# Optimization experiments

Hardware: AMD Instinct MI355X
Metric: run time of the kernel (lower is better)

## Reference

```python
import jax, jax.numpy as jnp
import numpy as np

B, C, H, W = 2, 256, 48, 48
HIDDEN, NUM_HEADS = 512, 8
HEAD_DIM = HIDDEN // NUM_HEADS
EPS = 1e-5


def setup_inputs() -> dict:
    key = jax.random.key(0)
    ks = jax.random.split(key, 16)
    inp = {
        'modal1_feat': jax.random.normal(ks[0], (B, C, H, W), jnp.float32),
        'modal2_feat': jax.random.normal(ks[1], (B, C, H, W), jnp.float32),
    }
    s = 0.02  # weight init scale
    names = ['wq1', 'wk1', 'wv1', 'wq2', 'wk2', 'wv2']
    for i, nm in enumerate(names):
        inp[nm] = jax.random.normal(ks[2 + i], (HIDDEN, C), jnp.float32) * s
        inp['b' + nm[1:]] = jnp.zeros((HIDDEN,), jnp.float32)
    inp['wo1'] = jax.random.normal(ks[8], (C, HIDDEN), jnp.float32) * s
    inp['bo1'] = jnp.zeros((C,), jnp.float32)
    inp['wo2'] = jax.random.normal(ks[9], (C, HIDDEN), jnp.float32) * s
    inp['bo2'] = jnp.zeros((C,), jnp.float32)
    inp['ln1_g'] = jnp.ones((C,), jnp.float32)
    inp['ln1_b'] = jnp.zeros((C,), jnp.float32)
    inp['ln2_g'] = jnp.ones((C,), jnp.float32)
    inp['ln2_b'] = jnp.zeros((C,), jnp.float32)
    inp['wf'] = jax.random.normal(ks[10], (C, 2 * C), jnp.float32) * s
    inp['bf'] = jnp.zeros((C,), jnp.float32)
    inp['bn_g'] = jnp.ones((C,), jnp.float32)
    inp['bn_b'] = jnp.zeros((C,), jnp.float32)
    inp['bn_mean'] = jnp.zeros((C,), jnp.float32)
    inp['bn_var'] = jnp.ones((C,), jnp.float32)
    return inp


def _conv1x1(x, w, b):
    return jnp.einsum('bchw,oc->bohw', x, w) + b[None, :, None, None]


def _ln_channels(x, g, b):
    # LayerNorm over channel dim (x: [B,C,H,W]) applied in NHWC layout
    xc = x.transpose(0, 2, 3, 1)
    mu = xc.mean(-1, keepdims=True)
    var = ((xc - mu) ** 2).mean(-1, keepdims=True)
    y = (xc - mu) / jnp.sqrt(var + EPS) * g + b
    return y.transpose(0, 3, 1, 2)


def reference(modal1_feat, modal2_feat, wq1, bq1, wk1, bk1, wv1, bv1,
              wq2, bq2, wk2, bk2, wv2, bv2, wo1, bo1, wo2, bo2,
              ln1_g, ln1_b, ln2_g, ln2_b, wf, bf, bn_g, bn_b, bn_mean, bn_var):
    b_, c1, h1, w1 = modal1_feat.shape
    hw = h1 * w1
    scale = HEAD_DIM ** -0.5

    def as_q(t):  # [B,hidden,H,W] -> [B,h,L,d]
        return t.reshape(b_, NUM_HEADS, HEAD_DIM, hw).transpose(0, 1, 3, 2)

    def as_k(t):  # [B,h,d,L]
        return t.reshape(b_, NUM_HEADS, HEAD_DIM, hw)

    q1 = as_q(_conv1x1(modal1_feat, wq1, bq1))
    k1 = as_k(_conv1x1(modal1_feat, wk1, bk1))
    v1 = as_q(_conv1x1(modal1_feat, wv1, bv1))
    q2 = as_q(_conv1x1(modal2_feat, wq2, bq2))
    k2 = as_k(_conv1x1(modal2_feat, wk2, bk2))
    v2 = as_q(_conv1x1(modal2_feat, wv2, bv2))

    a12 = jax.nn.softmax(jnp.einsum('bhld,bhdm->bhlm', q1, k2) * scale, axis=-1)
    o1 = jnp.einsum('bhlm,bhmd->bhld', a12, v2).transpose(0, 1, 3, 2).reshape(b_, HIDDEN, h1, w1)
    a21 = jax.nn.softmax(jnp.einsum('bhld,bhdm->bhlm', q2, k1) * scale, axis=-1)
    o2 = jnp.einsum('bhlm,bhmd->bhld', a21, v1).transpose(0, 1, 3, 2).reshape(b_, HIDDEN, h1, w1)

    mod1_cross = _conv1x1(o1, wo1, bo1)
    mod2_cross = _conv1x1(o2, wo2, bo2)

    m1 = _ln_channels(modal1_feat + mod1_cross, ln1_g, ln1_b)
    m2 = _ln_channels(modal2_feat + mod2_cross, ln2_g, ln2_b)

    fused = jnp.concatenate([m1, m2], axis=1)
    f = _conv1x1(fused, wf, bf)
    # BatchNorm2d in eval mode (running stats)
    f = (f - bn_mean[None, :, None, None]) / jnp.sqrt(bn_var + EPS)[None, :, None, None]
    f = f * bn_g[None, :, None, None] + bn_b[None, :, None, None]
    return jax.nn.relu(f)
```

## Files before the change

kernel.cpp:

```cpp
#include <hip/hip_runtime.h>
#include <hip/hip_bf16.h>

#define HW_N 2304
#define EPS_F 1e-5f
#define QSCALE 0.18033688011112043f

typedef float f32x4 __attribute__((ext_vector_type(4)));
typedef float f32x16 __attribute__((ext_vector_type(16)));
typedef unsigned u32x4 __attribute__((ext_vector_type(4)));
typedef short short8v __attribute__((ext_vector_type(8)));
typedef __bf16 bf16x8 __attribute__((ext_vector_type(8)));
typedef unsigned short u16;

__device__ __forceinline__ f32x4 mfma_bf16(bf16x8 a, bf16x8 b, f32x4 c) {
    return __builtin_amdgcn_mfma_f32_16x16x32_bf16(a, b, c, 0, 0, 0);
}
__device__ __forceinline__ f32x16 mfma32(bf16x8 a, bf16x8 b, f32x16 c) {
    return __builtin_amdgcn_mfma_f32_32x32x16_bf16(a, b, c, 0, 0, 0);
}
__device__ __forceinline__ bf16x8 ld8(const void* p) {
    return __builtin_bit_cast(bf16x8, *(const short8v*)p);
}
__device__ __forceinline__ unsigned short bfbits(float v) {
    return __builtin_bit_cast(unsigned short, __float2bfloat16(v));
}
__device__ __forceinline__ float b2f(u16 u) {
    unsigned x = (unsigned)u << 16;
    return __builtin_bit_cast(float, x);
}
__device__ __forceinline__ unsigned pack2(float lo, float hi) {
    return (unsigned)bfbits(lo) | ((unsigned)bfbits(hi) << 16);
}
__device__ __forceinline__ f32x16 zero16() {
    f32x16 z;
#pragma unroll
    for (int i = 0; i < 16; ++i) z[i] = 0.f;
    return z;
}

struct WPtrs { const float* s[9]; u16* d[9]; };

__global__ __launch_bounds__(256)
void conv_w_kernel(WPtrs p)
{
    const int j = blockIdx.z;
    const float* s = p.s[j];
    u16* d = p.d[j];
    const int i = (blockIdx.x * 256 + threadIdx.x) * 4;
    const float4 v = *(const float4*)(s + i);
    ushort4 pk;
    pk.x = bfbits(v.x); pk.y = bfbits(v.y); pk.z = bfbits(v.z); pk.w = bfbits(v.w);
    *(ushort4*)(d + i) = pk;
}

__global__ __launch_bounds__(256)
void prep_modal_kernel(const float* __restrict__ m1, const float* __restrict__ m2,
                       u16* __restrict__ t1, u16* __restrict__ t2)
{
    const int l0 = blockIdx.x * 64, c0 = blockIdx.y * 64;
    const int which = blockIdx.z >> 1, b = blockIdx.z & 1;
    const float* src = (which ? m2 : m1) + ((long long)b * 256 + c0) * HW_N + l0;
    u16* dst = (which ? t2 : t1) + ((long long)b * HW_N + l0) * 256 + c0;

    __shared__ float tile[64][65];
    const int t = threadIdx.x;
    const int r = t >> 4, cq = (t & 15) * 4;
#pragma unroll
    for (int i = 0; i < 4; ++i) {
        const int row = r + i * 16;
        const float4 v = *(const float4*)(src + (long long)row * HW_N + cq);
        tile[row][cq + 0] = v.x; tile[row][cq + 1] = v.y;
        tile[row][cq + 2] = v.z; tile[row][cq + 3] = v.w;
    }
    __syncthreads();
#pragma unroll
    for (int i = 0; i < 4; ++i) {
        const int lr = r + i * 16;
        ushort4 pk;
        pk.x = bfbits(tile[cq + 0][lr]);
        pk.y = bfbits(tile[cq + 1][lr]);
        pk.z = bfbits(tile[cq + 2][lr]);
        pk.w = bfbits(tile[cq + 3][lr]);
        *(ushort4*)(dst + (long long)lr * 256 + cq) = pk;
    }
}

struct GArgs {
    const u16* W[6];
    const float* bias[6];
    const u16* X[2];
    const u16* R[2];
    u16* outQ[2]; u16* outK[2]; u16* outV[2];
    float* outT[2];
    float* outC;
    const float *bnm, *bnv, *bng, *bnb;
};

template<int MODE>
__global__ __launch_bounds__(256)
void gemm_mfma(GArgs g)
{
    constexpr int KD = (MODE == 0) ? 256 : 512;
    constexpr int NS = KD / 32;
    const int z = blockIdx.y;
    const int j = blockIdx.z;
    const int mt_b = blockIdx.x / 18;
    const int nt_b = blockIdx.x - mt_b * 18;
    const int m0 = mt_b * 128, n0 = nt_b * 128;

    const u16* Wb = g.W[(MODE == 2) ? 0 : j];
    const u16* Xb0 = (MODE == 0) ? g.X[(j < 3) ? 0 : 1]
                                 : ((MODE == 1) ? g.X[j] : nullptr);

    __shared__ u16 Als[4096];
    __shared__ u16 Bls[4096];

    const int tid = threadIdx.x;
    const int w = tid >> 6, lane = tid & 63;
    const int l16 = lane & 15, lg = lane >> 4;

    const int ar0 = (((tid >> 6) << 4) | (tid & 15));
    const int k8 = (tid >> 4) & 3;

    short8v sa0, sa1, sb0, sb1;

    auto stage = [&](int kb) {
        const int koff = kb + k8 * 8;
        sa0 = *(const short8v*)(Wb + (long long)(m0 + ar0) * KD + koff);
        sa1 = *(const short8v*)(Wb + (long long)(m0 + ar0 + 64) * KD + koff);
        if constexpr (MODE == 0) {
            const u16* p = Xb0 + ((long long)z * HW_N + n0 + ar0) * 256 + koff;
            sb0 = *(const short8v*)p;
            sb1 = *(const short8v*)(p + 64LL * 256);
        } else if constexpr (MODE == 1) {
            const int head = kb >> 6;
            const u16* p = Xb0 + (((long long)z * 8 + head) * HW_N + n0 + ar0) * 64 + (koff & 63);
            sb0 = *(const short8v*)p;
            sb1 = *(const short8v*)(p + 64LL * 64);
        } else {
            const u16* Xb = (kb < 256) ? g.X[0] : g.X[1];
            const u16* p = Xb + ((long long)z * HW_N + n0 + ar0) * 256 + (koff & 255);
            sb0 = *(const short8v*)p;
            sb1 = *(const short8v*)(p + 64LL * 256);
        }
    };

    f32x4 acc[4][4];
#pragma unroll
    for (int a = 0; a < 4; ++a)
#pragma unroll
        for (int b = 0; b < 4; ++b) acc[a][b] = f32x4{0.f, 0.f, 0.f, 0.f};

    stage(0);
    for (int s = 0; s < NS; ++s) {
        __syncthreads();
        *(short8v*)((char*)Als + tid * 16) = sa0;
        *(short8v*)((char*)Als + tid * 16 + 4096) = sa1;
        *(short8v*)((char*)Bls + tid * 16) = sb0;
        *(short8v*)((char*)Bls + tid * 16 + 4096) = sb1;
        __syncthreads();
        if (s + 1 < NS) stage((s + 1) * 32);

        bf16x8 bfr[4];
#pragma unroll
        for (int nt = 0; nt < 4; ++nt)
            bfr[nt] = ld8((char*)Bls + ((w & 1) * 4 + nt) * 1024 + lane * 16);
#pragma unroll
        for (int mt = 0; mt < 4; ++mt) {
            const bf16x8 af = ld8((char*)Als + ((w >> 1) * 4 + mt) * 1024 + lane * 16);
#pragma unroll
            for (int nt = 0; nt < 4; ++nt)
                acc[mt][nt] = mfma_bf16(af, bfr[nt], acc[mt][nt]);
        }
    }

    const int mbase = m0 + (w >> 1) * 64 + 4 * lg;
    const int nbase = n0 + (w & 1) * 64 + l16;

    if constexpr (MODE == 0) {
        const int kind = j % 3, which = j / 3;
        const float* Bp = g.bias[j];
        if (kind < 2) {
            u16* T = (kind == 0) ? g.outQ[which] : g.outK[which];
            const float s = (kind == 0) ? QSCALE : 1.0f;
#pragma unroll
            for (int mt = 0; mt < 4; ++mt) {
                const int m = mbase + mt * 16;
                const float4 bv = *(const float4*)(Bp + m);
#pragma unroll
                for (int nt = 0; nt < 4; ++nt) {
                    const int l = nbase + nt * 16;
                    const f32x4 a = acc[mt][nt];
                    ushort4 pk;
                    pk.x = bfbits((a.x + bv.x) * s);
                    pk.y = bfbits((a.y + bv.y) * s);
                    pk.z = bfbits((a.z + bv.z) * s);
                    pk.w = bfbits((a.w + bv.w) * s);
                    *(ushort4*)(T + ((long long)(z * 8 + (m >> 6)) * HW_N + l) * 64 + (m & 63)) = pk;
                }
            }
        } else {
            u16* V = g.outV[which];
#pragma unroll
            for (int mt = 0; mt < 4; ++mt) {
                const int m = mbase + mt * 16;
                const float4 bv = *(const float4*)(Bp + m);
#pragma unroll
                for (int nt = 0; nt < 4; ++nt) {
                    const int l = nbase + nt * 16;
                    const f32x4 a = acc[mt][nt];
                    V[((long long)z * 512 + m + 0) * HW_N + l] = bfbits(a.x + bv.x);
                    V[((long long)z * 512 + m + 1) * HW_N + l] = bfbits(a.y + bv.y);
                    V[((long long)z * 512 + m + 2) * HW_N + l] = bfbits(a.z + bv.z);
                    V[((long long)z * 512 + m + 3) * HW_N + l] = bfbits(a.w + bv.w);
                }
            }
        }
    } else if constexpr (MODE == 1) {
        const float* Bp = g.bias[j];
        const u16* Rb = g.R[j];
        float* Ob = g.outT[j];
#pragma unroll
        for (int mt = 0; mt < 4; ++mt) {
            const int m = mbase + mt * 16;
            const float4 bv = *(const float4*)(Bp + m);
#pragma unroll
            for (int nt = 0; nt < 4; ++nt) {
                const int l = nbase + nt * 16;
                const long long rowoff = ((long long)z * HW_N + l) * 256 + m;
                const ushort4 rv = *(const ushort4*)(Rb + rowoff);
                const f32x4 a = acc[mt][nt];
                float4 o;
                o.x = a.x + bv.x + b2f(rv.x);
                o.y = a.y + bv.y + b2f(rv.y);
                o.z = a.z + bv.z + b2f(rv.z);
                o.w = a.w + bv.w + b2f(rv.w);
                *(float4*)(Ob + rowoff) = o;
            }
        }
    } else {
        const float* Bp = g.bias[0];
#pragma unroll
        for (int mt = 0; mt < 4; ++mt) {
            const int m = mbase + mt * 16;
            const float4 bv = *(const float4*)(Bp + m);
            const float4 mu = *(const float4*)(g.bnm + m);
            const float4 vr = *(const float4*)(g.bnv + m);
            const float4 ga = *(const float4*)(g.bng + m);
            const float4 be = *(const float4*)(g.bnb + m);
            const float sc0 = ga.x * rsqrtf(vr.x + EPS_F), sh0 = be.x - mu.x * sc0;
            const float sc1 = ga.y * rsqrtf(vr.y + EPS_F), sh1 = be.y - mu.y * sc1;
            const float sc2 = ga.z * rsqrtf(vr.z + EPS_F), sh2 = be.z - mu.z * sc2;
            const float sc3 = ga.w * rsqrtf(vr.w + EPS_F), sh3 = be.w - mu.w * sc3;
#pragma unroll
            for (int nt = 0; nt < 4; ++nt) {
                const int l = nbase + nt * 16;
                const f32x4 a = acc[mt][nt];
                float* O = g.outC + (long long)z * 256 * HW_N + l;
                O[(long long)(m + 0) * HW_N] = fmaxf((a.x + bv.x) * sc0 + sh0, 0.f);
                O[(long long)(m + 1) * HW_N] = fmaxf((a.y + bv.y) * sc1 + sh1, 0.f);
                O[(long long)(m + 2) * HW_N] = fmaxf((a.z + bv.z) * sc2 + sh2, 0.f);
                O[(long long)(m + 3) * HW_N] = fmaxf((a.w + bv.w) * sc3 + sh3, 0.f);
            }
        }
    }
}

__global__ __launch_bounds__(256)
void attn_mfma_kernel(const u16* __restrict__ qt0, const u16* __restrict__ kt0,
                      const u16* __restrict__ v0b,
                      const u16* __restrict__ qt1, const u16* __restrict__ kt1,
                      const u16* __restrict__ v1b,
                      u16* __restrict__ oat0T, u16* __restrict__ oat1T)
{
    const int flat = blockIdx.x;
    const int virt = (flat & 7) * 72 + (flat >> 3);
    const int lt = virt % 18;
    const int hz = virt / 18;
    const int h = hz & 7;
    const int zz = hz >> 3;
    const int b = zz >> 1, dir = zz & 1;

    const u16* QT = dir ? qt1 : qt0;
    const u16* KT = dir ? kt0 : kt1;
    const u16* V  = dir ? v0b : v1b;

    const long long bh = (long long)(b * 8 + h);
    const u16* Qb = QT + bh * HW_N * 64;
    const u16* Kb = KT + bh * HW_N * 64;
    const u16* Vb = V + ((long long)b * 512 + h * 64) * HW_N;

    const int tid = threadIdx.x;
    const int w = tid >> 6, lane = tid & 63;
    const int l32 = lane & 31, hi = lane >> 5;
    const int q0 = lt * 128 + w * 32;

    __shared__ u16 Ks[2][64 * 64];
    __shared__ u16 Vs[2][64 * 64];

    bf16x8 qf0, qf1, qf2, qf3;
    {
        const u16* qrow = Qb + (long long)(q0 + l32) * 64 + 8 * hi;
        qf0 = ld8(qrow);       qf1 = ld8(qrow + 16);
        qf2 = ld8(qrow + 32);  qf3 = ld8(qrow + 48);
    }
    bf16x8 onesv;
    {
        short8v o;
#pragma unroll
        for (int i = 0; i < 8; ++i) o[i] = (short)0x3F80;
        onesv = __builtin_bit_cast(bf16x8, o);
    }

    f32x16 accA = zero16(), accB = zero16(), accs = zero16();
    float m_run = -1e30f;

    auto SWZ = [](int r) { return ((r ^ (r >> 3)) & 7) << 4; };

    const int rsub = lane >> 3;
    const int csub = (lane & 7) * 8;
    const int r0 = 16 * w + rsub, r1 = r0 + 8;
    const int swz0 = (csub * 2) ^ SWZ(r0);
    const int swz1 = (csub * 2) ^ SWZ(r1);

    short8v ka, kb2, va, vb2;
    auto stage = [&](int t) {
        const int m0 = t * 64;
        const u16* kbase = Kb + (long long)(m0 + 16 * w) * 64;
        ka  = *(const short8v*)(kbase + (long long)rsub * 64 + csub);
        kb2 = *(const short8v*)(kbase + (long long)(8 + rsub) * 64 + csub);
        const u16* vbase = Vb + (long long)(16 * w + rsub) * HW_N + m0 + csub;
        va  = *(const short8v*)(vbase);
        vb2 = *(const short8v*)(vbase + 8LL * HW_N);
    };
    auto commit = [&](int buf) {
        *(short8v*)((char*)Ks[buf] + r0 * 128 + swz0) = ka;
        *(short8v*)((char*)Ks[buf] + r1 * 128 + swz1) = kb2;
        *(short8v*)((char*)Vs[buf] + r0 * 128 + swz0) = va;
        *(short8v*)((char*)Vs[buf] + r1 * 128 + swz1) = vb2;
    };

    const int rb0 = l32 * 128;
    const int rb1 = (l32 + 32) * 128;
    const int cs0 = (16 * hi) ^ SWZ(l32);
    const int cs1 = (16 * hi) ^ SWZ(l32 + 32);

    stage(0); commit(0); stage(1);
    __syncthreads();

    for (int t = 0; t < 36; ++t) {
        const int cur = t & 1;
        const char* kbase = (const char*)Ks[cur];
        const char* vbase = (const char*)Vs[cur];

        const bf16x8 kf00 = ld8(kbase + rb0 + (cs0 ^ 0));
        const bf16x8 kf01 = ld8(kbase + rb1 + (cs1 ^ 0));
        const bf16x8 kf10 = ld8(kbase + rb0 + (cs0 ^ 32));
        const bf16x8 kf11 = ld8(kbase + rb1 + (cs1 ^ 32));
        const bf16x8 kf20 = ld8(kbase + rb0 + (cs0 ^ 64));
        const bf16x8 kf21 = ld8(kbase + rb1 + (cs1 ^ 64));
        const bf16x8 kf30 = ld8(kbase + rb0 + (cs0 ^ 96));
        const bf16x8 kf31 = ld8(kbase + rb1 + (cs1 ^ 96));

        if (t + 1 < 36) commit(cur ^ 1);
        if (t + 2 < 36) stage(t + 2);

        f32x16 s0 = zero16(), s1 = zero16();
        __builtin_amdgcn_s_setprio(1);
        s0 = mfma32(kf00, qf0, s0); s1 = mfma32(kf01, qf0, s1);
        s0 = mfma32(kf10, qf1, s0); s1 = mfma32(kf11, qf1, s1);
        s0 = mfma32(kf20, qf2, s0); s1 = mfma32(kf21, qf2, s1);
        s0 = mfma32(kf30, qf3, s0); s1 = mfma32(kf31, qf3, s1);
        __builtin_amdgcn_s_setprio(0);

        const bf16x8 vf00 = ld8(vbase + rb0 + (cs0 ^ 0));
        const bf16x8 vf01 = ld8(vbase + rb1 + (cs1 ^ 0));
        const bf16x8 vf10 = ld8(vbase + rb0 + (cs0 ^ 32));
        const bf16x8 vf11 = ld8(vbase + rb1 + (cs1 ^ 32));
        const bf16x8 vf20 = ld8(vbase + rb0 + (cs0 ^ 64));
        const bf16x8 vf21 = ld8(vbase + rb1 + (cs1 ^ 64));
        const bf16x8 vf30 = ld8(vbase + rb0 + (cs0 ^ 96));
        const bf16x8 vf31 = ld8(vbase + rb1 + (cs1 ^ 96));

        f32x16 mv;
#pragma unroll
        for (int i = 0; i < 16; ++i) mv[i] = fmaxf(s0[i], s1[i]);
        float ma = fmaxf(fmaxf(mv[0], mv[1]), fmaxf(mv[2], mv[3]));
        float mb = fmaxf(fmaxf(mv[4], mv[5]), fmaxf(mv[6], mv[7]));
        float mc = fmaxf(fmaxf(mv[8], mv[9]), fmaxf(mv[10], mv[11]));
        float md = fmaxf(fmaxf(mv[12], mv[13]), fmaxf(mv[14], mv[15]));
        float mx = fmaxf(fmaxf(ma, mb), fmaxf(mc, md));
        {
            unsigned mu = __builtin_bit_cast(unsigned, mx);
            unsigned mv2 = mu;
            asm("v_permlane32_swap_b32 %0, %1" : "+v"(mu), "+v"(mv2));
            mx = fmaxf(__builtin_bit_cast(float, mu), __builtin_bit_cast(float, mv2));
        }

        if (!__all(mx <= m_run + 8.f)) {
            const float m_new = fmaxf(m_run, mx);
            const float alpha = exp2f(m_run - m_new);
#pragma unroll
            for (int i = 0; i < 16; ++i) {
                accA[i] *= alpha; accB[i] *= alpha; accs[i] *= alpha;
            }
            m_run = m_new;
        }

#pragma unroll
        for (int i = 0; i < 16; ++i) {
            s0[i] = exp2f(s0[i] - m_run);
            s1[i] = exp2f(s1[i] - m_run);
        }

        __builtin_amdgcn_s_setprio(1);
#define PVSTEP(S, PT, VF0, VF1) { \
        constexpr int qe = 2 * ((S) & 1), qo = qe + 1; \
        unsigned a0 = pack2(PT[4 * qe + 0], PT[4 * qe + 1]); \
        unsigned b0 = pack2(PT[4 * qe + 2], PT[4 * qe + 3]); \
        unsigned a1 = pack2(PT[4 * qo + 0], PT[4 * qo + 1]); \
        unsigned b1 = pack2(PT[4 * qo + 2], PT[4 * qo + 3]); \
        asm("v_permlane32_swap_b32 %0, %1" : "+v"(a0), "+v"(a1)); \
        asm("v_permlane32_swap_b32 %0, %1" : "+v"(b0), "+v"(b1)); \
        u32x4 pw = {a0, b0, a1, b1}; \
        const bf16x8 pf = __builtin_bit_cast(bf16x8, pw); \
        accA = mfma32(VF0, pf, accA); \
        accB = mfma32(VF1, pf, accB); \
        accs = mfma32(onesv, pf, accs); }
        PVSTEP(0, s0, vf00, vf01)
        PVSTEP(1, s0, vf10, vf11)
        PVSTEP(2, s1, vf20, vf21)
        PVSTEP(3, s1, vf30, vf31)
#undef PVSTEP
        __builtin_amdgcn_s_setprio(0);

        __syncthreads();
    }

    const float inv = 1.0f / accs[0];
    u16* obase = (dir ? oat1T : oat0T) + (bh * HW_N + q0 + l32) * 64;
#pragma unroll
    for (int g = 0; g < 4; ++g) {
        ushort4 pk;
        pk.x = bfbits(accA[4 * g + 0] * inv);
        pk.y = bfbits(accA[4 * g + 1] * inv);
        pk.z = bfbits(accA[4 * g + 2] * inv);
        pk.w = bfbits(accA[4 * g + 3] * inv);
        *(ushort4*)(obase + 8 * g + 4 * hi) = pk;
        pk.x = bfbits(accB[4 * g + 0] * inv);
        pk.y = bfbits(accB[4 * g + 1] * inv);
        pk.z = bfbits(accB[4 * g + 2] * inv);
        pk.w = bfbits(accB[4 * g + 3] * inv);
        *(ushort4*)(obase + 32 + 8 * g + 4 * hi) = pk;
    }
}

__global__ __launch_bounds__(256)
void ln_t_kernel(const float* __restrict__ mpre0T, const float* __restrict__ mpre1T,
                 const float* __restrict__ g1, const float* __restrict__ b1,
                 const float* __restrict__ g2, const float* __restrict__ b2,
                 u16* __restrict__ mln0T, u16* __restrict__ mln1T)
{
    const int l = blockIdx.x * 64 + (threadIdx.x >> 2);
    const int z = blockIdx.y, dir = blockIdx.z;
    const float* src = (dir ? mpre1T : mpre0T) + ((long long)z * HW_N + l) * 256;
    const float* gg = dir ? g2 : g1;
    const float* bb = dir ? b2 : b1;
    u16* dst = (dir ? mln1T : mln0T) + ((long long)z * HW_N + l) * 256;
    const int q = (threadIdx.x & 3) * 64;

    float4 vbuf[16];
    float sum = 0.f, sq = 0.f;
#pragma unroll
    for (int i = 0; i < 16; ++i) {
        const float4 v = *(const float4*)(src + q + i * 4);
        vbuf[i] = v;
        sum += (v.x + v.y) + (v.z + v.w);
        sq += (v.x * v.x + v.y * v.y) + (v.z * v.z + v.w * v.w);
    }
    sum += __shfl_xor(sum, 1, 64); sum += __shfl_xor(sum, 2, 64);
    sq  += __shfl_xor(sq, 1, 64);  sq  += __shfl_xor(sq, 2, 64);
    const float mean = sum * (1.f / 256.f);
    const float var = sq * (1.f / 256.f) - mean * mean;
    const float rstd = rsqrtf(var + EPS_F);
#pragma unroll
    for (int i = 0; i < 16; ++i) {
        const int c = q + i * 4;
        const float4 gv = *(const float4*)(gg + c);
        const float4 bv = *(const float4*)(bb + c);
        ushort4 pk;
        pk.x = bfbits((vbuf[i].x - mean) * rstd * gv.x + bv.x);
        pk.y = bfbits((vbuf[i].y - mean) * rstd * gv.y + bv.y);
        pk.z = bfbits((vbuf[i].z - mean) * rstd * gv.z + bv.z);
        pk.w = bfbits((vbuf[i].w - mean) * rstd * gv.w + bv.w);
        *(ushort4*)(dst + c) = pk;
    }
}

extern "C" void kernel_launch(void* const* d_in, const int* in_sizes, int n_in,
                              void* d_out, int out_size, void* d_ws, size_t ws_size,
                              hipStream_t stream)
{
    (void)in_sizes; (void)n_in; (void)out_size; (void)ws_size;

    const float* modal1 = (const float*)d_in[0];
    const float* modal2 = (const float*)d_in[1];
    const float* wqkv[6]; const float* bqkv[6];
    for (int j = 0; j < 6; ++j) {
        wqkv[j] = (const float*)d_in[2 + 2 * j];
        bqkv[j] = (const float*)d_in[3 + 2 * j];
    }
    const float* wo1 = (const float*)d_in[14];
    const float* bo1 = (const float*)d_in[15];
    const float* wo2 = (const float*)d_in[16];
    const float* bo2 = (const float*)d_in[17];
    const float* ln1_g = (const float*)d_in[18];
    const float* ln1_b = (const float*)d_in[19];
    const float* ln2_g = (const float*)d_in[20];
    const float* ln2_b = (const float*)d_in[21];
    const float* wf = (const float*)d_in[22];
    const float* bf = (const float*)d_in[23];
    const float* bn_g = (const float*)d_in[24];
    const float* bn_b = (const float*)d_in[25];
    const float* bn_mean = (const float*)d_in[26];
    const float* bn_var = (const float*)d_in[27];

    char* ws = (char*)d_ws;
    size_t off = 0;
    auto alloc = [&](size_t bytes) { char* p = ws + off; off += (bytes + 255) & ~(size_t)255; return p; };

    u16* modalT[2]; u16* wbf[9]; u16* qT[2]; u16* kT[2]; u16* vC[2];
    u16* oatT[2]; float* mpreT[2]; u16* mlnT[2];
    for (int i = 0; i < 2; ++i) modalT[i] = (u16*)alloc(2LL * HW_N * 256 * 2);
    for (int i = 0; i < 9; ++i) wbf[i] = (u16*)alloc(131072 * 2);
    for (int i = 0; i < 2; ++i) qT[i] = (u16*)alloc(2LL * 512 * HW_N * 2);
    for (int i = 0; i < 2; ++i) kT[i] = (u16*)alloc(2LL * 512 * HW_N * 2);
    for (int i = 0; i < 2; ++i) vC[i] = (u16*)alloc(2LL * 512 * HW_N * 2);
    for (int i = 0; i < 2; ++i) oatT[i] = (u16*)alloc(2LL * 512 * HW_N * 2);
    for (int i = 0; i < 2; ++i) mpreT[i] = (float*)alloc(2LL * HW_N * 256 * 4);
    for (int i = 0; i < 2; ++i) mlnT[i] = (u16*)alloc(2LL * HW_N * 256 * 2);

    WPtrs wp;
    for (int j = 0; j < 6; ++j) { wp.s[j] = wqkv[j]; wp.d[j] = wbf[j]; }
    wp.s[6] = wo1; wp.d[6] = wbf[6];
    wp.s[7] = wo2; wp.d[7] = wbf[7];
    wp.s[8] = wf;  wp.d[8] = wbf[8];
    conv_w_kernel<<<dim3(128, 1, 9), 256, 0, stream>>>(wp);
    prep_modal_kernel<<<dim3(36, 4, 4), 256, 0, stream>>>(modal1, modal2, modalT[0], modalT[1]);

    GArgs g0 = {};
    for (int j = 0; j < 6; ++j) { g0.W[j] = wbf[j]; g0.bias[j] = bqkv[j]; }
    g0.X[0] = modalT[0]; g0.X[1] = modalT[1];
    for (int i = 0; i < 2; ++i) { g0.outQ[i] = qT[i]; g0.outK[i] = kT[i]; g0.outV[i] = vC[i]; }
    gemm_mfma<0><<<dim3(72, 2, 6), 256, 0, stream>>>(g0);

    attn_mfma_kernel<<<dim3(576), 256, 0, stream>>>(
        qT[0], kT[0], vC[0], qT[1], kT[1], vC[1], oatT[0], oatT[1]);

    GArgs g1a = {};
    g1a.W[0] = wbf[6]; g1a.W[1] = wbf[7];
    g1a.bias[0] = bo1; g1a.bias[1] = bo2;
    g1a.X[0] = oatT[0]; g1a.X[1] = oatT[1];
    g1a.R[0] = modalT[0]; g1a.R[1] = modalT[1];
    g1a.outT[0] = mpreT[0]; g1a.outT[1] = mpreT[1];
    gemm_mfma<1><<<dim3(36, 2, 2), 256, 0, stream>>>(g1a);

    ln_t_kernel<<<dim3(36, 2, 2), 256, 0, stream>>>(
        mpreT[0], mpreT[1], ln1_g, ln1_b, ln2_g, ln2_b, mlnT[0], mlnT[1]);

    GArgs g2a = {};
    g2a.W[0] = wbf[8]; g2a.bias[0] = bf;
    g2a.X[0] = mlnT[0]; g2a.X[1] = mlnT[1];
    g2a.outC = (float*)d_out;
    g2a.bnm = bn_mean; g2a.bnv = bn_var; g2a.bng = bn_g; g2a.bnb = bn_b;
    gemm_mfma<2><<<dim3(36, 2, 1), 256, 0, stream>>>(g2a);
}
```

Before: 187.9 us.

## Split attention KV range in two and merge partials in combine kernel

Splits each attention tile's 36 KV steps into two halves handled by separate blocks, doubling the grid from 576 to 1152 blocks, which fills the GPU's compute units more evenly. Each block writes unnormalized fp32 partial outputs plus its running max and sum. A new combine kernel rescales the two halves and writes the normalized bf16 output. This costs extra fp32 partial traffic and one more launch. The later mpre/mln buffers are aliased onto the partial region to save workspace, and launch_bounds adds a min-blocks hint.

```diff
diff --git a/kernel.cpp b/kernel.cpp
--- a/kernel.cpp
+++ b/kernel.cpp
@@ -266,20 +266,24 @@
     }
 }
 
-__global__ __launch_bounds__(256)
+__global__ __launch_bounds__(256, 4)
 void attn_mfma_kernel(const u16* __restrict__ qt0, const u16* __restrict__ kt0,
                       const u16* __restrict__ v0b,
                       const u16* __restrict__ qt1, const u16* __restrict__ kt1,
                       const u16* __restrict__ v1b,
-                      u16* __restrict__ oat0T, u16* __restrict__ oat1T)
+                      float* __restrict__ PO, float* __restrict__ PM,
+                      float* __restrict__ PS)
 {
     const int flat = blockIdx.x;
-    const int virt = (flat & 7) * 72 + (flat >> 3);
+    const int virt = (flat & 7) * 144 + (flat >> 3);
     const int lt = virt % 18;
-    const int hz = virt / 18;
-    const int h = hz & 7;
-    const int zz = hz >> 3;
+    const int rest = virt / 18;
+    const int h = rest & 7;
+    const int zz2 = rest >> 3;
+    const int zz = zz2 & 3;
+    const int sp = zz2 >> 2;
     const int b = zz >> 1, dir = zz & 1;
+    const int t0 = sp * 18;
 
     const u16* QT = dir ? qt1 : qt0;
     const u16* KT = dir ? kt0 : kt1;
@@ -345,10 +349,10 @@
     const int cs0 = (16 * hi) ^ SWZ(l32);
     const int cs1 = (16 * hi) ^ SWZ(l32 + 32);
 
-    stage(0); commit(0); stage(1);
+    stage(t0); commit(0); stage(t0 + 1);
     __syncthreads();
 
-    for (int t = 0; t < 36; ++t) {
+    for (int t = 0; t < 18; ++t) {
         const int cur = t & 1;
         const char* kbase = (const char*)Ks[cur];
         const char* vbase = (const char*)Vs[cur];
@@ -362,8 +366,8 @@
         const bf16x8 kf30 = ld8(kbase + rb0 + (cs0 ^ 96));
         const bf16x8 kf31 = ld8(kbase + rb1 + (cs1 ^ 96));
 
-        if (t + 1 < 36) commit(cur ^ 1);
-        if (t + 2 < 36) stage(t + 2);
+        if (t + 1 < 18) commit(cur ^ 1);
+        if (t + 2 < 18) stage(t0 + t + 2);
 
         f32x16 s0 = zero16(), s1 = zero16();
         __builtin_amdgcn_s_setprio(1);
@@ -437,21 +441,58 @@
         __syncthreads();
     }
 
-    const float inv = 1.0f / accs[0];
-    u16* obase = (dir ? oat1T : oat0T) + (bh * HW_N + q0 + l32) * 64;
+    const long long prow = ((long long)sp * 32 + (zz * 8 + h)) * HW_N + q0 + l32;
+    float* POr = PO + prow * 64;
 #pragma unroll
     for (int g = 0; g < 4; ++g) {
+        float4 o;
+        o.x = accA[4 * g + 0]; o.y = accA[4 * g + 1];
+        o.z = accA[4 * g + 2]; o.w = accA[4 * g + 3];
+        *(float4*)(POr + 8 * g + 4 * hi) = o;
+        o.x = accB[4 * g + 0]; o.y = accB[4 * g + 1];
+        o.z = accB[4 * g + 2]; o.w = accB[4 * g + 3];
+        *(float4*)(POr + 32 + 8 * g + 4 * hi) = o;
+    }
+    if (hi == 0) {
+        PM[prow] = m_run;
+        PS[prow] = accs[0];
+    }
+}
+
+__global__ __launch_bounds__(256)
+void attn_combine_kernel(const float* __restrict__ PO, const float* __restrict__ PM,
+                         const float* __restrict__ PS,
+                         u16* __restrict__ oat0T, u16* __restrict__ oat1T)
+{
+    const int bhh = blockIdx.y;
+    const int q = blockIdx.x * 64 + (threadIdx.x >> 2);
+    const int d0 = (threadIdx.x & 3) * 16;
+    const long long row = (long long)bhh * HW_N + q;
+    const long long MS = 32LL * HW_N;
+    const long long POS = MS * 64;
+
+    const float m0 = PM[row], m1 = PM[MS + row];
+    const float s0 = PS[row], s1 = PS[MS + row];
+    const float mm = fmaxf(m0, m1);
+    const float a0 = exp2f(m0 - mm), a1 = exp2f(m1 - mm);
+    const float inv = 1.0f / (s0 * a0 + s1 * a1);
+    const float w0 = a0 * inv, w1 = a1 * inv;
+
+    const float* p0 = PO + row * 64 + d0;
+    const float* p1 = p0 + POS;
+    const int zz = bhh >> 3, h = bhh & 7;
+    const int b = zz >> 1, dir = zz & 1;
+    u16* out = (dir ? oat1T : oat0T) + ((long long)(b * 8 + h) * HW_N + q) * 64 + d0;
+#pragma unroll
+    for (int i = 0; i < 4; ++i) {
+        const float4 v0 = *(const float4*)(p0 + 4 * i);
+        const float4 v1 = *(const float4*)(p1 + 4 * i);
         ushort4 pk;
-        pk.x = bfbits(accA[4 * g + 0] * inv);
-        pk.y = bfbits(accA[4 * g + 1] * inv);
-        pk.z = bfbits(accA[4 * g + 2] * inv);
-        pk.w = bfbits(accA[4 * g + 3] * inv);
-        *(ushort4*)(obase + 8 * g + 4 * hi) = pk;
-        pk.x = bfbits(accB[4 * g + 0] * inv);
-        pk.y = bfbits(accB[4 * g + 1] * inv);
-        pk.z = bfbits(accB[4 * g + 2] * inv);
-        pk.w = bfbits(accB[4 * g + 3] * inv);
-        *(ushort4*)(obase + 32 + 8 * g + 4 * hi) = pk;
+        pk.x = bfbits(v0.x * w0 + v1.x * w1);
+        pk.y = bfbits(v0.y * w0 + v1.y * w1);
+        pk.z = bfbits(v0.z * w0 + v1.z * w1);
+        pk.w = bfbits(v0.w * w0 + v1.w * w1);
+        *(ushort4*)(out + 4 * i) = pk;
     }
 }
 
@@ -530,15 +571,25 @@
     auto alloc = [&](size_t bytes) { char* p = ws + off; off += (bytes + 255) & ~(size_t)255; return p; };
 
     u16* modalT[2]; u16* wbf[9]; u16* qT[2]; u16* kT[2]; u16* vC[2];
-    u16* oatT[2]; float* mpreT[2]; u16* mlnT[2];
+    u16* oatT[2];
     for (int i = 0; i < 2; ++i) modalT[i] = (u16*)alloc(2LL * HW_N * 256 * 2);
     for (int i = 0; i < 9; ++i) wbf[i] = (u16*)alloc(131072 * 2);
     for (int i = 0; i < 2; ++i) qT[i] = (u16*)alloc(2LL * 512 * HW_N * 2);
     for (int i = 0; i < 2; ++i) kT[i] = (u16*)alloc(2LL * 512 * HW_N * 2);
     for (int i = 0; i < 2; ++i) vC[i] = (u16*)alloc(2LL * 512 * HW_N * 2);
     for (int i = 0; i < 2; ++i) oatT[i] = (u16*)alloc(2LL * 512 * HW_N * 2);
-    for (int i = 0; i < 2; ++i) mpreT[i] = (float*)alloc(2LL * HW_N * 256 * 4);
-    for (int i = 0; i < 2; ++i) mlnT[i] = (u16*)alloc(2LL * HW_N * 256 * 2);
+
+    const size_t PO_BYTES = 2LL * 32 * HW_N * 64 * 4;
+    const size_t PMS_BYTES = 2LL * 32 * HW_N * 4;
+    char* region = alloc(PO_BYTES + 2 * PMS_BYTES);
+    float* PO = (float*)region;
+    float* PM = (float*)(region + PO_BYTES);
+    float* PS = (float*)(region + PO_BYTES + PMS_BYTES);
+    float* mpreT[2]; u16* mlnT[2];
+    mpreT[0] = (float*)region;
+    mpreT[1] = (float*)(region + 2LL * HW_N * 256 * 4);
+    mlnT[0] = (u16*)(region + 4LL * HW_N * 256 * 4);
+    mlnT[1] = (u16*)(region + 4LL * HW_N * 256 * 4 + 2LL * HW_N * 256 * 2);
 
     WPtrs wp;
     for (int j = 0; j < 6; ++j) { wp.s[j] = wqkv[j]; wp.d[j] = wbf[j]; }
@@ -554,8 +605,9 @@
     for (int i = 0; i < 2; ++i) { g0.outQ[i] = qT[i]; g0.outK[i] = kT[i]; g0.outV[i] = vC[i]; }
     gemm_mfma<0><<<dim3(72, 2, 6), 256, 0, stream>>>(g0);
 
-    attn_mfma_kernel<<<dim3(576), 256, 0, stream>>>(
-        qT[0], kT[0], vC[0], qT[1], kT[1], vC[1], oatT[0], oatT[1]);
+    attn_mfma_kernel<<<dim3(1152), 256, 0, stream>>>(
+        qT[0], kT[0], vC[0], qT[1], kT[1], vC[1], PO, PM, PS);
+    attn_combine_kernel<<<dim3(36, 32), 256, 0, stream>>>(PO, PM, PS, oatT[0], oatT[1]);
 
     GArgs g1a = {};
     g1a.W[0] = wbf[6]; g1a.W[1] = wbf[7];
```

Result: slower. 321.4 us (+71.0%).
